# Optimization experiments

Hardware: AMD Instinct MI355X
Metric: run time of the kernel (lower is better)

The kernel has to match this reference:

```python
import jax, jax.numpy as jnp
import numpy as np

B, S, D, H = 4, 2048, 1024, 16
DH = D // H  # 64


def setup_inputs() -> dict:
    key = jax.random.key(0)
    ks = jax.random.split(key, 7)
    scale = 1.0 / np.sqrt(DH)  # ~ torch Linear init scale
    return {
        "seqs": jax.random.normal(ks[0], (B, S, D), dtype=jnp.float32),
        "Wq": jax.random.normal(ks[1], (H, DH, DH), dtype=jnp.float32) * scale,
        "bq": jax.random.normal(ks[2], (H, DH), dtype=jnp.float32) * scale,
        "Wk": jax.random.normal(ks[3], (H, DH, DH), dtype=jnp.float32) * scale,
        "bk": jax.random.normal(ks[4], (H, DH), dtype=jnp.float32) * scale,
        "Wv": jax.random.normal(ks[5], (H, DH, DH), dtype=jnp.float32) * scale,
        "bv": jax.random.normal(ks[6], (H, DH), dtype=jnp.float32) * scale,
    }


def reference(seqs, Wq, bq, Wk, bk, Wv, bv):
    # seqs: [B, S, D] -> per-head slices [B, S, H, DH]
    x = seqs.reshape(B, S, H, DH)
    # torch Linear: y = s @ W.T + b  (W: [out, in]) -> einsum over 'in' axis d
    q = jnp.einsum("bshd,hed->bshe", x, Wq) + bq  # [B,S,H,DH]
    k = jnp.einsum("bshd,hed->bshe", x, Wk) + bk
    v = jnp.einsum("bshd,hed->bshe", x, Wv) + bv
    inv_sqrt = 1.0 / jnp.sqrt(jnp.asarray(DH, dtype=seqs.dtype))
    scores = jnp.einsum("bshe,bthe->bhst", q, k) * inv_sqrt  # [B,H,S,S]
    attn = jax.nn.softmax(scores, axis=-1)
    out = jnp.einsum("bhst,bthe->bshe", attn, v)  # [B,S,H,DH]
    # torch.hstack over heads == concat along feature dim
    return out.reshape(B, S, D)
```

## Files before the change

### kernel.cpp

```cpp
#include <hip/hip_runtime.h>
#include <hip/hip_bf16.h>

#define NB 4
#define NS 2048
#define ND 1024
#define NH 16
#define NDH 64
#define KT 64
#define SCF 0.18033688011112042f

typedef __attribute__((ext_vector_type(8))) short bf16x8;
typedef __attribute__((ext_vector_type(4))) float f32x4;

__device__ __forceinline__ float bf2f(unsigned short u) {
    union { unsigned int u; float f; } x; x.u = ((unsigned int)u) << 16; return x.f;
}
__device__ __forceinline__ unsigned short f2bf(float f) {
    union { float f; unsigned int u; } x; x.f = f;
    unsigned int r = x.u + 0x7FFFu + ((x.u >> 16) & 1u);
    return (unsigned short)(r >> 16);
}
__device__ __forceinline__ unsigned short f2bf_fast(float f) {
    union { float f; unsigned int u; } x; x.f = f;
    return (unsigned short)((x.u + 0x8000u) >> 16);
}
__device__ __forceinline__ unsigned int pkbf(float a, float b) {
    union { float f; unsigned int u; } x, y; x.f = a; y.f = b;
    return __builtin_amdgcn_perm(y.u + 0x8000u, x.u + 0x8000u, 0x07060302u);
}
__device__ __forceinline__ unsigned int pktr(float a, float b) {
    union { float f; unsigned int u; } x, y; x.f = a; y.f = b;
    return __builtin_amdgcn_perm(y.u, x.u, 0x07060302u);
}

__global__ __launch_bounds__(256) void convert_w_kernel(
    const unsigned short* __restrict__ x,
    const void* __restrict__ Wq, const void* __restrict__ bq,
    const void* __restrict__ Wk, const void* __restrict__ bk,
    const void* __restrict__ Wv, const void* __restrict__ bv,
    int* __restrict__ flag,
    unsigned short* __restrict__ Wb,
    unsigned short* __restrict__ Bb)
{
    __shared__ int sflag;
    const int tid = threadIdx.x;
    if (tid < 64) {
        int bad = 0, zer = 0;
        for (int i = tid; i < 1024; i += 64) {
            const unsigned short u = x[2 * i];
            const int e = (u >> 7) & 0xFF;
            if (e >= 0x8F) bad++;
            if (e == 0 && (u & 0x7F)) bad++;
            if (u == 0) zer++;
        }
        #pragma unroll
        for (int off = 1; off < 64; off <<= 1) {
            bad += __shfl_xor(bad, off, 64);
            zer += __shfl_xor(zer, off, 64);
        }
        if (tid == 0) {
            const int f = (bad > 64 || zer > 512) ? 1 : 0;
            sflag = f;
            flag[0] = f;
        }
    }
    __syncthreads();
    const int isf32 = sflag;

    const void* Wsrc[3] = { Wq, Wk, Wv };
    const void* Bsrc[3] = { bq, bk, bv };
    const int NW = 3 * 65536, NBIAS = 3 * 1024;
    for (int i = blockIdx.x * blockDim.x + tid; i < NW + NBIAS;
         i += gridDim.x * blockDim.x) {
        int m, off; const void* src; unsigned short* dst;
        if (i < NW) { m = i >> 16; off = i & 65535; src = Wsrc[m]; dst = Wb + i; }
        else { int j = i - NW; m = j >> 10; off = j & 1023; src = Bsrc[m];
               dst = Bb + j; }
        float v = isf32 ? ((const float*)src)[off]
                        : bf2f(((const unsigned short*)src)[off]);
        if (m == 0) v *= SCF;
        *dst = f2bf(v);
    }
}

__global__ __launch_bounds__(256) void qkv_proj_kernel(
    const unsigned short* __restrict__ x,
    const unsigned short* __restrict__ Wb,
    const unsigned short* __restrict__ Bb,
    const int* __restrict__ flag,
    unsigned short* __restrict__ Qw, unsigned short* __restrict__ Kw,
    unsigned short* __restrict__ VwT)
{
    __shared__ __align__(16) unsigned short Tl[3 * 64 * 72];

    const int isf32 = flag[0];
    const int tid  = threadIdx.x;
    const int wave = tid >> 6, lane = tid & 63;
    const int quad = lane >> 4, l16 = lane & 15;
    const int ttile = blockIdx.x;
    const int h     = blockIdx.y;
    const int b  = ttile >> 5;
    const int s0 = (ttile & 31) * 64;
    const int bh = b * NH + h;

    const int tok_a = ttile * 64 + wave * 16 + l16;
    bf16x8 af0, af1;
    if (isf32) {
        const f32x4* xp = (const f32x4*)((const float*)x + (size_t)tok_a * ND + h * NDH);
        const f32x4 v0 = xp[quad * 2], v1 = xp[quad * 2 + 1];
        const f32x4 v2 = xp[8 + quad * 2], v3 = xp[8 + quad * 2 + 1];
        union { bf16x8 v; unsigned int d[4]; } a0, a1;
        a0.d[0] = pkbf(v0[0], v0[1]); a0.d[1] = pkbf(v0[2], v0[3]);
        a0.d[2] = pkbf(v1[0], v1[1]); a0.d[3] = pkbf(v1[2], v1[3]);
        a1.d[0] = pkbf(v2[0], v2[1]); a1.d[1] = pkbf(v2[2], v2[3]);
        a1.d[2] = pkbf(v3[0], v3[1]); a1.d[3] = pkbf(v3[2], v3[3]);
        af0 = a0.v; af1 = a1.v;
    } else {
        const unsigned short* xr = x + (size_t)tok_a * ND + h * NDH;
        af0 = *(const bf16x8*)(xr + quad * 8);
        af1 = *(const bf16x8*)(xr + 32 + quad * 8);
    }

    #pragma unroll
    for (int m = 0; m < 3; ++m) {
        const unsigned short* W = Wb + m * 65536 + h * 4096;
        unsigned short* R = Tl + m * (64 * 72);
        #pragma unroll
        for (int n = 0; n < 4; ++n) {
            const unsigned short* wrow = W + (n * 16 + l16) * NDH;
            const bf16x8 b0 = *(const bf16x8*)(wrow + quad * 8);
            const bf16x8 b1 = *(const bf16x8*)(wrow + 32 + quad * 8);
            f32x4 acc = {0.f, 0.f, 0.f, 0.f};
            acc = __builtin_amdgcn_mfma_f32_16x16x32_bf16(af0, b0, acc, 0, 0, 0);
            acc = __builtin_amdgcn_mfma_f32_16x16x32_bf16(af1, b1, acc, 0, 0, 0);
            const float bias = bf2f(Bb[m * 1024 + h * NDH + n * 16 + l16]);
            if (m < 2) {
                #pragma unroll
                for (int r = 0; r < 4; ++r) {
                    const int row = wave * 16 + quad * 4 + r;
                    R[row * 72 + n * 16 + l16] = f2bf_fast(acc[r] + bias);
                }
            } else {
                #pragma unroll
                for (int r = 0; r < 4; ++r) {
                    const int tok = wave * 16 + quad * 4 + r;
                    const int pc = ((tok & 15) << 2) | (tok >> 4);
                    R[(n * 16 + l16) * 72 + pc] = f2bf_fast(acc[r] + bias);
                }
            }
        }
    }
    __syncthreads();
    #pragma unroll
    for (int p = 0; p < 2; ++p) {
        const int ch = tid + p * 256;
        const int tl = ch >> 3, sub = ch & 7;
        *(bf16x8*)(Qw + ((size_t)bh * NS + s0 + tl) * NDH + sub * 8) =
            *(const bf16x8*)(Tl + tl * 72 + sub * 8);
        *(bf16x8*)(Kw + ((size_t)bh * NS + s0 + tl) * NDH + sub * 8) =
            *(const bf16x8*)(Tl + 64 * 72 + tl * 72 + sub * 8);
        *(bf16x8*)(VwT + ((size_t)bh * NDH + tl) * NS + s0 + sub * 8) =
            *(const bf16x8*)(Tl + 2 * 64 * 72 + tl * 72 + sub * 8);
    }
}

__global__ __launch_bounds__(256, 4) void attn_kernel(
    const unsigned short* __restrict__ Qw,
    const unsigned short* __restrict__ Kw,
    const unsigned short* __restrict__ VwT,
    const int* __restrict__ flag,
    unsigned short* __restrict__ out)
{
    __shared__ __align__(16) unsigned short smem[(64 + 64 + 128) * 72];
    unsigned short* Kt = smem;
    unsigned short* Vt = smem + 64 * 72;
    unsigned short* Pt = smem + 128 * 72;
    unsigned short* Ot = smem;

    const int isf32 = flag[0];
    const int tid  = threadIdx.x;
    const int wave = tid >> 6, lane = tid & 63;
    const int quad = lane >> 4, l16 = lane & 15;
    const int qt = blockIdx.x & 15;
    const int bh = blockIdx.x >> 4;
    const int b = bh >> 4, h = bh & 15;

    const unsigned short* Qb = Qw  + (size_t)bh * NS * NDH;
    const unsigned short* Kb = Kw  + (size_t)bh * NS * NDH;
    const unsigned short* Vb = VwT + (size_t)bh * NDH * NS;

    bf16x8 qf[2][2];
    #pragma unroll
    for (int mh = 0; mh < 2; ++mh) {
        const int tok = qt * 128 + wave * 32 + mh * 16 + l16;
        qf[mh][0] = *(const bf16x8*)(Qb + (size_t)tok * NDH + quad * 8);
        qf[mh][1] = *(const bf16x8*)(Qb + (size_t)tok * NDH + 32 + quad * 8);
    }

    bf16x8 ones_b;
    {
        const short v = (l16 == 0) ? (short)0x3F80 : (short)0;
        #pragma unroll
        for (int j = 0; j < 8; ++j) ones_b[j] = v;
    }

    f32x4 o[2][4], os[2];
    #pragma unroll
    for (int mh = 0; mh < 2; ++mh) {
        #pragma unroll
        for (int n = 0; n < 4; ++n) o[mh][n] = f32x4{0.f, 0.f, 0.f, 0.f};
        os[mh] = f32x4{0.f, 0.f, 0.f, 0.f};
    }

    const int stage_r = tid >> 3, stage_c = tid & 7;
    unsigned short* PtW = Pt + wave * (32 * 72);

    for (int kt = 0; kt < NS / KT; ++kt) {
        __syncthreads();
        #pragma unroll
        for (int p = 0; p < 2; ++p) {
            const int rr = stage_r + p * 32;
            *(bf16x8*)(Kt + rr * 72 + stage_c * 8) =
                *(const bf16x8*)(Kb + (size_t)(kt * KT + rr) * NDH + stage_c * 8);
            *(bf16x8*)(Vt + rr * 72 + stage_c * 8) =
                *(const bf16x8*)(Vb + (size_t)rr * NS + kt * KT + stage_c * 8);
        }
        __syncthreads();

        f32x4 sf[2][4];
        #pragma unroll
        for (int n = 0; n < 4; ++n) {
            const bf16x8 kb0 = *(const bf16x8*)(Kt + (n * 16 + l16) * 72 + quad * 8);
            const bf16x8 kb1 = *(const bf16x8*)(Kt + (n * 16 + l16) * 72 + 32 + quad * 8);
            #pragma unroll
            for (int mh = 0; mh < 2; ++mh) {
                f32x4 acc = {0.f, 0.f, 0.f, 0.f};
                acc = __builtin_amdgcn_mfma_f32_16x16x32_bf16(qf[mh][0], kb0, acc, 0, 0, 0);
                acc = __builtin_amdgcn_mfma_f32_16x16x32_bf16(qf[mh][1], kb1, acc, 0, 0, 0);
                sf[mh][n] = acc;
            }
        }

        #pragma unroll
        for (int mh = 0; mh < 2; ++mh) {
            #pragma unroll
            for (int r = 0; r < 4; ++r) {
                const float p0 = __builtin_amdgcn_exp2f(sf[mh][0][r]);
                const float p1 = __builtin_amdgcn_exp2f(sf[mh][1][r]);
                const float p2 = __builtin_amdgcn_exp2f(sf[mh][2][r]);
                const float p3 = __builtin_amdgcn_exp2f(sf[mh][3][r]);
                uint2 d; d.x = pktr(p0, p1); d.y = pktr(p2, p3);
                *(uint2*)(PtW + (mh * 16 + quad * 4 + r) * 72 + l16 * 4) = d;
            }
        }

        bf16x8 pa[2][2];
        #pragma unroll
        for (int mh = 0; mh < 2; ++mh) {
            pa[mh][0] = *(const bf16x8*)(PtW + (mh * 16 + l16) * 72 + quad * 8);
            pa[mh][1] = *(const bf16x8*)(PtW + (mh * 16 + l16) * 72 + 32 + quad * 8);
        }

        #pragma unroll
        for (int n = 0; n < 4; ++n) {
            const bf16x8 vb0 = *(const bf16x8*)(Vt + (n * 16 + l16) * 72 + quad * 8);
            const bf16x8 vb1 = *(const bf16x8*)(Vt + (n * 16 + l16) * 72 + 32 + quad * 8);
            #pragma unroll
            for (int mh = 0; mh < 2; ++mh) {
                o[mh][n] = __builtin_amdgcn_mfma_f32_16x16x32_bf16(pa[mh][0], vb0, o[mh][n], 0, 0, 0);
                o[mh][n] = __builtin_amdgcn_mfma_f32_16x16x32_bf16(pa[mh][1], vb1, o[mh][n], 0, 0, 0);
            }
        }
        #pragma unroll
        for (int mh = 0; mh < 2; ++mh) {
            os[mh] = __builtin_amdgcn_mfma_f32_16x16x32_bf16(pa[mh][0], ones_b, os[mh], 0, 0, 0);
            os[mh] = __builtin_amdgcn_mfma_f32_16x16x32_bf16(pa[mh][1], ones_b, os[mh], 0, 0, 0);
        }
    }

    float inv[2][4];
    #pragma unroll
    for (int mh = 0; mh < 2; ++mh)
        #pragma unroll
        for (int r = 0; r < 4; ++r)
            inv[mh][r] = 1.0f / __shfl(os[mh][r], lane & 48, 64);

    if (isf32) {
        float* of = (float*)out;
        #pragma unroll
        for (int mh = 0; mh < 2; ++mh) {
            #pragma unroll
            for (int r = 0; r < 4; ++r) {
                const int s = qt * 128 + wave * 32 + mh * 16 + quad * 4 + r;
                #pragma unroll
                for (int n = 0; n < 4; ++n)
                    of[((size_t)(b * NS + s)) * ND + h * NDH + n * 16 + l16] =
                        o[mh][n][r] * inv[mh][r];
            }
        }
    } else {
        __syncthreads();
        #pragma unroll
        for (int mh = 0; mh < 2; ++mh) {
            #pragma unroll
            for (int r = 0; r < 4; ++r) {
                const int row = wave * 32 + mh * 16 + quad * 4 + r;
                #pragma unroll
                for (int n = 0; n < 4; ++n)
                    Ot[row * 72 + n * 16 + l16] = f2bf(o[mh][n][r] * inv[mh][r]);
            }
        }
        __syncthreads();
        #pragma unroll
        for (int p = 0; p < 4; ++p) {
            const int ch = tid + p * 256;
            const int tl = ch >> 3, sub = ch & 7;
            const int s = qt * 128 + tl;
            *(bf16x8*)(out + ((size_t)(b * NS + s)) * ND + h * NDH + sub * 8) =
                *(const bf16x8*)(Ot + tl * 72 + sub * 8);
        }
    }
}

extern "C" void kernel_launch(void* const* d_in, const int* in_sizes, int n_in,
                              void* d_out, int out_size, void* d_ws, size_t ws_size,
                              hipStream_t stream)
{
    const unsigned short* x = (const unsigned short*)d_in[0];
    int* flag = (int*)d_ws;
    const size_t per = (size_t)NB * NH * NS * NDH;
    unsigned short* Qw  = (unsigned short*)((char*)d_ws + 256);
    unsigned short* Kw  = Qw + per;
    unsigned short* VwT = Kw + per;
    unsigned short* Wb  = VwT + per;
    unsigned short* Bb  = Wb + 3 * 65536;

    convert_w_kernel<<<256, 256, 0, stream>>>(
        x, d_in[1], d_in[2], d_in[3], d_in[4], d_in[5], d_in[6], flag, Wb, Bb);
    qkv_proj_kernel<<<dim3(NB * NS / 64, NH), 256, 0, stream>>>(
        x, Wb, Bb, flag, Qw, Kw, VwT);
    attn_kernel<<<NB * NH * (NS / 128), 256, 0, stream>>>(
        Qw, Kw, VwT, flag, (unsigned short*)d_out);
}
```

Before: 209.4 us.

## Fuse weight conversion into projection and double-buffer larger attention tiles

Removes the separate weight-conversion kernel: each projection block now converts and scales the weights on the fly and detects the input dtype itself. The attention kernel doubles the query tile to 256 rows per block (64 per wave), double-buffers the K/V tiles in shared memory, and prefetches the next tile into registers. This cuts one launch and K/V reloads per query, at the cost of more registers, lower occupancy (launch bounds 2), and redundant dtype detection and weight conversion in every block.

```diff
diff --git a/kernel.cpp b/kernel.cpp
--- a/kernel.cpp
+++ b/kernel.cpp
@@ -6,7 +6,6 @@
 #define ND 1024
 #define NH 16
 #define NDH 64
-#define KT 64
 #define SCF 0.18033688011112042f
 
 typedef __attribute__((ext_vector_type(8))) short bf16x8;
@@ -33,17 +32,9 @@
     return __builtin_amdgcn_perm(y.u, x.u, 0x07060302u);
 }
 
-__global__ __launch_bounds__(256) void convert_w_kernel(
-    const unsigned short* __restrict__ x,
-    const void* __restrict__ Wq, const void* __restrict__ bq,
-    const void* __restrict__ Wk, const void* __restrict__ bk,
-    const void* __restrict__ Wv, const void* __restrict__ bv,
-    int* __restrict__ flag,
-    unsigned short* __restrict__ Wb,
-    unsigned short* __restrict__ Bb)
+__device__ __forceinline__ int detect_f32(const unsigned short* x, int tid,
+                                          int* sflag)
 {
-    __shared__ int sflag;
-    const int tid = threadIdx.x;
     if (tid < 64) {
         int bad = 0, zer = 0;
         for (int i = tid; i < 1024; i += 64) {
@@ -58,47 +49,28 @@
             bad += __shfl_xor(bad, off, 64);
             zer += __shfl_xor(zer, off, 64);
         }
-        if (tid == 0) {
-            const int f = (bad > 64 || zer > 512) ? 1 : 0;
-            sflag = f;
-            flag[0] = f;
-        }
+        if (tid == 0) *sflag = (bad > 64 || zer > 512) ? 1 : 0;
     }
     __syncthreads();
-    const int isf32 = sflag;
-
-    const void* Wsrc[3] = { Wq, Wk, Wv };
-    const void* Bsrc[3] = { bq, bk, bv };
-    const int NW = 3 * 65536, NBIAS = 3 * 1024;
-    for (int i = blockIdx.x * blockDim.x + tid; i < NW + NBIAS;
-         i += gridDim.x * blockDim.x) {
-        int m, off; const void* src; unsigned short* dst;
-        if (i < NW) { m = i >> 16; off = i & 65535; src = Wsrc[m]; dst = Wb + i; }
-        else { int j = i - NW; m = j >> 10; off = j & 1023; src = Bsrc[m];
-               dst = Bb + j; }
-        float v = isf32 ? ((const float*)src)[off]
-                        : bf2f(((const unsigned short*)src)[off]);
-        if (m == 0) v *= SCF;
-        *dst = f2bf(v);
-    }
+    return *sflag;
 }
 
 __global__ __launch_bounds__(256) void qkv_proj_kernel(
     const unsigned short* __restrict__ x,
-    const unsigned short* __restrict__ Wb,
-    const unsigned short* __restrict__ Bb,
-    const int* __restrict__ flag,
+    const void* __restrict__ Wq, const void* __restrict__ bq,
+    const void* __restrict__ Wk, const void* __restrict__ bk,
+    const void* __restrict__ Wv, const void* __restrict__ bv,
     unsigned short* __restrict__ Qw, unsigned short* __restrict__ Kw,
     unsigned short* __restrict__ VwT)
 {
     __shared__ __align__(16) unsigned short Tl[3 * 64 * 72];
-
-    const int isf32 = flag[0];
+    __shared__ int sflag;
+
     const int tid  = threadIdx.x;
+    const int isf32 = detect_f32(x, tid, &sflag);
     const int wave = tid >> 6, lane = tid & 63;
     const int quad = lane >> 4, l16 = lane & 15;
-    const int ttile = blockIdx.x;
-    const int h     = blockIdx.y;
+    const int ttile = blockIdx.x, h = blockIdx.y;
     const int b  = ttile >> 5;
     const int s0 = (ttile & 31) * 64;
     const int bh = b * NH + h;
@@ -121,19 +93,52 @@
         af1 = *(const bf16x8*)(xr + 32 + quad * 8);
     }
 
+    const void* Wsrc[3] = { Wq, Wk, Wv };
+    const void* Bsrc[3] = { bq, bk, bv };
+
     #pragma unroll
     for (int m = 0; m < 3; ++m) {
-        const unsigned short* W = Wb + m * 65536 + h * 4096;
         unsigned short* R = Tl + m * (64 * 72);
         #pragma unroll
         for (int n = 0; n < 4; ++n) {
-            const unsigned short* wrow = W + (n * 16 + l16) * NDH;
-            const bf16x8 b0 = *(const bf16x8*)(wrow + quad * 8);
-            const bf16x8 b1 = *(const bf16x8*)(wrow + 32 + quad * 8);
+            bf16x8 b0, b1;
+            if (isf32) {
+                const float* wrow = (const float*)Wsrc[m] + h * 4096
+                                    + (n * 16 + l16) * NDH;
+                const f32x4* wp = (const f32x4*)wrow;
+                f32x4 w0 = wp[quad * 2], w1 = wp[quad * 2 + 1];
+                f32x4 w2 = wp[8 + quad * 2], w3 = wp[8 + quad * 2 + 1];
+                if (m == 0) {
+                    #pragma unroll
+                    for (int j = 0; j < 4; ++j) {
+                        w0[j] *= SCF; w1[j] *= SCF; w2[j] *= SCF; w3[j] *= SCF;
+                    }
+                }
+                union { bf16x8 v; unsigned int d[4]; } t0, t1;
+                t0.d[0] = pkbf(w0[0], w0[1]); t0.d[1] = pkbf(w0[2], w0[3]);
+                t0.d[2] = pkbf(w1[0], w1[1]); t0.d[3] = pkbf(w1[2], w1[3]);
+                t1.d[0] = pkbf(w2[0], w2[1]); t1.d[1] = pkbf(w2[2], w2[3]);
+                t1.d[2] = pkbf(w3[0], w3[1]); t1.d[3] = pkbf(w3[2], w3[3]);
+                b0 = t0.v; b1 = t1.v;
+            } else {
+                const unsigned short* wrow = (const unsigned short*)Wsrc[m]
+                                             + h * 4096 + (n * 16 + l16) * NDH;
+                b0 = *(const bf16x8*)(wrow + quad * 8);
+                b1 = *(const bf16x8*)(wrow + 32 + quad * 8);
+                if (m == 0) {
+                    #pragma unroll
+                    for (int j = 0; j < 8; ++j) {
+                        b0[j] = (short)f2bf(bf2f((unsigned short)b0[j]) * SCF);
+                        b1[j] = (short)f2bf(bf2f((unsigned short)b1[j]) * SCF);
+                    }
+                }
+            }
             f32x4 acc = {0.f, 0.f, 0.f, 0.f};
             acc = __builtin_amdgcn_mfma_f32_16x16x32_bf16(af0, b0, acc, 0, 0, 0);
             acc = __builtin_amdgcn_mfma_f32_16x16x32_bf16(af1, b1, acc, 0, 0, 0);
-            const float bias = bf2f(Bb[m * 1024 + h * NDH + n * 16 + l16]);
+            float bias = isf32 ? ((const float*)Bsrc[m])[h * NDH + n * 16 + l16]
+                               : bf2f(((const unsigned short*)Bsrc[m])[h * NDH + n * 16 + l16]);
+            if (m == 0) bias *= SCF;
             if (m < 2) {
                 #pragma unroll
                 for (int r = 0; r < 4; ++r) {
@@ -164,35 +169,34 @@
     }
 }
 
-__global__ __launch_bounds__(256, 4) void attn_kernel(
+__global__ __launch_bounds__(256, 2) void attn_kernel(
+    const unsigned short* __restrict__ xdet,
     const unsigned short* __restrict__ Qw,
     const unsigned short* __restrict__ Kw,
     const unsigned short* __restrict__ VwT,
-    const int* __restrict__ flag,
     unsigned short* __restrict__ out)
 {
-    __shared__ __align__(16) unsigned short smem[(64 + 64 + 128) * 72];
-    unsigned short* Kt = smem;
-    unsigned short* Vt = smem + 64 * 72;
-    unsigned short* Pt = smem + 128 * 72;
+    __shared__ __align__(16) unsigned short smem[8 * 64 * 72];
+    __shared__ int sflag;
+    unsigned short* Pt = smem + 4 * 64 * 72;
     unsigned short* Ot = smem;
 
-    const int isf32 = flag[0];
     const int tid  = threadIdx.x;
+    const int isf32 = detect_f32(xdet, tid, &sflag);
     const int wave = tid >> 6, lane = tid & 63;
     const int quad = lane >> 4, l16 = lane & 15;
-    const int qt = blockIdx.x & 15;
-    const int bh = blockIdx.x >> 4;
+    const int qt = blockIdx.x & 7;
+    const int bh = blockIdx.x >> 3;
     const int b = bh >> 4, h = bh & 15;
 
     const unsigned short* Qb = Qw  + (size_t)bh * NS * NDH;
     const unsigned short* Kb = Kw  + (size_t)bh * NS * NDH;
     const unsigned short* Vb = VwT + (size_t)bh * NDH * NS;
 
-    bf16x8 qf[2][2];
-    #pragma unroll
-    for (int mh = 0; mh < 2; ++mh) {
-        const int tok = qt * 128 + wave * 32 + mh * 16 + l16;
+    bf16x8 qf[4][2];
+    #pragma unroll
+    for (int mh = 0; mh < 4; ++mh) {
+        const int tok = qt * 256 + wave * 64 + mh * 16 + l16;
         qf[mh][0] = *(const bf16x8*)(Qb + (size_t)tok * NDH + quad * 8);
         qf[mh][1] = *(const bf16x8*)(Qb + (size_t)tok * NDH + 32 + quad * 8);
     }
@@ -204,83 +208,94 @@
         for (int j = 0; j < 8; ++j) ones_b[j] = v;
     }
 
-    f32x4 o[2][4], os[2];
-    #pragma unroll
-    for (int mh = 0; mh < 2; ++mh) {
+    f32x4 o[4][4], os[4];
+    #pragma unroll
+    for (int mh = 0; mh < 4; ++mh) {
         #pragma unroll
         for (int n = 0; n < 4; ++n) o[mh][n] = f32x4{0.f, 0.f, 0.f, 0.f};
         os[mh] = f32x4{0.f, 0.f, 0.f, 0.f};
     }
 
     const int stage_r = tid >> 3, stage_c = tid & 7;
-    unsigned short* PtW = Pt + wave * (32 * 72);
-
-    for (int kt = 0; kt < NS / KT; ++kt) {
-        __syncthreads();
+    unsigned short* PtW = Pt + wave * (64 * 72);
+
+    bf16x8 kpre[2], vpre[2];
+    #pragma unroll
+    for (int p = 0; p < 2; ++p) {
+        const int rr = stage_r + p * 32;
+        kpre[p] = *(const bf16x8*)(Kb + (size_t)rr * NDH + stage_c * 8);
+        vpre[p] = *(const bf16x8*)(Vb + (size_t)rr * NS + stage_c * 8);
+    }
+
+    for (int kt = 0; kt < NS / 64; ++kt) {
+        unsigned short* KB = smem + (kt & 1) * (64 * 72);
+        unsigned short* VB = smem + (2 + (kt & 1)) * (64 * 72);
         #pragma unroll
         for (int p = 0; p < 2; ++p) {
             const int rr = stage_r + p * 32;
-            *(bf16x8*)(Kt + rr * 72 + stage_c * 8) =
-                *(const bf16x8*)(Kb + (size_t)(kt * KT + rr) * NDH + stage_c * 8);
-            *(bf16x8*)(Vt + rr * 72 + stage_c * 8) =
-                *(const bf16x8*)(Vb + (size_t)rr * NS + kt * KT + stage_c * 8);
+            *(bf16x8*)(KB + rr * 72 + stage_c * 8) = kpre[p];
+            *(bf16x8*)(VB + rr * 72 + stage_c * 8) = vpre[p];
         }
         __syncthreads();
-
-        f32x4 sf[2][4];
+        if (kt + 1 < NS / 64) {
+            #pragma unroll
+            for (int p = 0; p < 2; ++p) {
+                const int rr = stage_r + p * 32;
+                kpre[p] = *(const bf16x8*)(Kb + (size_t)((kt + 1) * 64 + rr) * NDH + stage_c * 8);
+                vpre[p] = *(const bf16x8*)(Vb + (size_t)rr * NS + (kt + 1) * 64 + stage_c * 8);
+            }
+        }
+
+        bf16x8 kb[4][2];
         #pragma unroll
         for (int n = 0; n < 4; ++n) {
-            const bf16x8 kb0 = *(const bf16x8*)(Kt + (n * 16 + l16) * 72 + quad * 8);
-            const bf16x8 kb1 = *(const bf16x8*)(Kt + (n * 16 + l16) * 72 + 32 + quad * 8);
-            #pragma unroll
-            for (int mh = 0; mh < 2; ++mh) {
+            kb[n][0] = *(const bf16x8*)(KB + (n * 16 + l16) * 72 + quad * 8);
+            kb[n][1] = *(const bf16x8*)(KB + (n * 16 + l16) * 72 + 32 + quad * 8);
+        }
+        #pragma unroll
+        for (int mh = 0; mh < 4; ++mh) {
+            f32x4 sf[4];
+            #pragma unroll
+            for (int n = 0; n < 4; ++n) {
                 f32x4 acc = {0.f, 0.f, 0.f, 0.f};
-                acc = __builtin_amdgcn_mfma_f32_16x16x32_bf16(qf[mh][0], kb0, acc, 0, 0, 0);
-                acc = __builtin_amdgcn_mfma_f32_16x16x32_bf16(qf[mh][1], kb1, acc, 0, 0, 0);
-                sf[mh][n] = acc;
-            }
-        }
-
-        #pragma unroll
-        for (int mh = 0; mh < 2; ++mh) {
+                acc = __builtin_amdgcn_mfma_f32_16x16x32_bf16(qf[mh][0], kb[n][0], acc, 0, 0, 0);
+                acc = __builtin_amdgcn_mfma_f32_16x16x32_bf16(qf[mh][1], kb[n][1], acc, 0, 0, 0);
+                sf[n] = acc;
+            }
             #pragma unroll
             for (int r = 0; r < 4; ++r) {
-                const float p0 = __builtin_amdgcn_exp2f(sf[mh][0][r]);
-                const float p1 = __builtin_amdgcn_exp2f(sf[mh][1][r]);
-                const float p2 = __builtin_amdgcn_exp2f(sf[mh][2][r]);
-                const float p3 = __builtin_amdgcn_exp2f(sf[mh][3][r]);
+                const float p0 = __builtin_amdgcn_exp2f(sf[0][r]);
+                const float p1 = __builtin_amdgcn_exp2f(sf[1][r]);
+                const float p2 = __builtin_amdgcn_exp2f(sf[2][r]);
+                const float p3 = __builtin_amdgcn_exp2f(sf[3][r]);
                 uint2 d; d.x = pktr(p0, p1); d.y = pktr(p2, p3);
                 *(uint2*)(PtW + (mh * 16 + quad * 4 + r) * 72 + l16 * 4) = d;
             }
         }
 
-        bf16x8 pa[2][2];
-        #pragma unroll
-        for (int mh = 0; mh < 2; ++mh) {
-            pa[mh][0] = *(const bf16x8*)(PtW + (mh * 16 + l16) * 72 + quad * 8);
-            pa[mh][1] = *(const bf16x8*)(PtW + (mh * 16 + l16) * 72 + 32 + quad * 8);
-        }
-
+        bf16x8 vb[4][2];
         #pragma unroll
         for (int n = 0; n < 4; ++n) {
-            const bf16x8 vb0 = *(const bf16x8*)(Vt + (n * 16 + l16) * 72 + quad * 8);
-            const bf16x8 vb1 = *(const bf16x8*)(Vt + (n * 16 + l16) * 72 + 32 + quad * 8);
-            #pragma unroll
-            for (int mh = 0; mh < 2; ++mh) {
-                o[mh][n] = __builtin_amdgcn_mfma_f32_16x16x32_bf16(pa[mh][0], vb0, o[mh][n], 0, 0, 0);
-                o[mh][n] = __builtin_amdgcn_mfma_f32_16x16x32_bf16(pa[mh][1], vb1, o[mh][n], 0, 0, 0);
-            }
-        }
-        #pragma unroll
-        for (int mh = 0; mh < 2; ++mh) {
-            os[mh] = __builtin_amdgcn_mfma_f32_16x16x32_bf16(pa[mh][0], ones_b, os[mh], 0, 0, 0);
-            os[mh] = __builtin_amdgcn_mfma_f32_16x16x32_bf16(pa[mh][1], ones_b, os[mh], 0, 0, 0);
-        }
-    }
-
-    float inv[2][4];
-    #pragma unroll
-    for (int mh = 0; mh < 2; ++mh)
+            vb[n][0] = *(const bf16x8*)(VB + (n * 16 + l16) * 72 + quad * 8);
+            vb[n][1] = *(const bf16x8*)(VB + (n * 16 + l16) * 72 + 32 + quad * 8);
+        }
+        #pragma unroll
+        for (int mh = 0; mh < 4; ++mh) {
+            const bf16x8 pa0 = *(const bf16x8*)(PtW + (mh * 16 + l16) * 72 + quad * 8);
+            const bf16x8 pa1 = *(const bf16x8*)(PtW + (mh * 16 + l16) * 72 + 32 + quad * 8);
+            #pragma unroll
+            for (int n = 0; n < 4; ++n) {
+                o[mh][n] = __builtin_amdgcn_mfma_f32_16x16x32_bf16(pa0, vb[n][0], o[mh][n], 0, 0, 0);
+                o[mh][n] = __builtin_amdgcn_mfma_f32_16x16x32_bf16(pa1, vb[n][1], o[mh][n], 0, 0, 0);
+            }
+            os[mh] = __builtin_amdgcn_mfma_f32_16x16x32_bf16(pa0, ones_b, os[mh], 0, 0, 0);
+            os[mh] = __builtin_amdgcn_mfma_f32_16x16x32_bf16(pa1, ones_b, os[mh], 0, 0, 0);
+        }
+    }
+
+    float inv[4][4];
+    #pragma unroll
+    for (int mh = 0; mh < 4; ++mh)
         #pragma unroll
         for (int r = 0; r < 4; ++r)
             inv[mh][r] = 1.0f / __shfl(os[mh][r], lane & 48, 64);
@@ -288,10 +303,10 @@
     if (isf32) {
         float* of = (float*)out;
         #pragma unroll
-        for (int mh = 0; mh < 2; ++mh) {
+        for (int mh = 0; mh < 4; ++mh) {
             #pragma unroll
             for (int r = 0; r < 4; ++r) {
-                const int s = qt * 128 + wave * 32 + mh * 16 + quad * 4 + r;
+                const int s = qt * 256 + wave * 64 + mh * 16 + quad * 4 + r;
                 #pragma unroll
                 for (int n = 0; n < 4; ++n)
                     of[((size_t)(b * NS + s)) * ND + h * NDH + n * 16 + l16] =
@@ -301,10 +316,10 @@
     } else {
         __syncthreads();
         #pragma unroll
-        for (int mh = 0; mh < 2; ++mh) {
+        for (int mh = 0; mh < 4; ++mh) {
             #pragma unroll
             for (int r = 0; r < 4; ++r) {
-                const int row = wave * 32 + mh * 16 + quad * 4 + r;
+                const int row = wave * 64 + mh * 16 + quad * 4 + r;
                 #pragma unroll
                 for (int n = 0; n < 4; ++n)
                     Ot[row * 72 + n * 16 + l16] = f2bf(o[mh][n][r] * inv[mh][r]);
@@ -312,10 +327,10 @@
         }
         __syncthreads();
         #pragma unroll
-        for (int p = 0; p < 4; ++p) {
+        for (int p = 0; p < 8; ++p) {
             const int ch = tid + p * 256;
             const int tl = ch >> 3, sub = ch & 7;
-            const int s = qt * 128 + tl;
+            const int s = qt * 256 + tl;
             *(bf16x8*)(out + ((size_t)(b * NS + s)) * ND + h * NDH + sub * 8) =
                 *(const bf16x8*)(Ot + tl * 72 + sub * 8);
         }
@@ -327,18 +342,13 @@
                               hipStream_t stream)
 {
     const unsigned short* x = (const unsigned short*)d_in[0];
-    int* flag = (int*)d_ws;
     const size_t per = (size_t)NB * NH * NS * NDH;
-    unsigned short* Qw  = (unsigned short*)((char*)d_ws + 256);
+    unsigned short* Qw  = (unsigned short*)d_ws;
     unsigned short* Kw  = Qw + per;
     unsigned short* VwT = Kw + per;
-    unsigned short* Wb  = VwT + per;
-    unsigned short* Bb  = Wb + 3 * 65536;
-
-    convert_w_kernel<<<256, 256, 0, stream>>>(
-        x, d_in[1], d_in[2], d_in[3], d_in[4], d_in[5], d_in[6], flag, Wb, Bb);
+
     qkv_proj_kernel<<<dim3(NB * NS / 64, NH), 256, 0, stream>>>(
-        x, Wb, Bb, flag, Qw, Kw, VwT);
-    attn_kernel<<<NB * NH * (NS / 128), 256, 0, stream>>>(
-        Qw, Kw, VwT, flag, (unsigned short*)d_out);
-}
+        x, d_in[1], d_in[2], d_in[3], d_in[4], d_in[5], d_in[6], Qw, Kw, VwT);
+    attn_kernel<<<NB * NH * (NS / 256), 256, 0, stream>>>(
+        x, Qw, Kw, VwT, (unsigned short*)d_out);
+}
```

Result: slower. 221.1 us (+5.6%).
